# Kernel optimization log

Measured on AMD Instinct MI355X. Metric: run time of the kernel, lower is better.

Reference implementation:

```python
import jax, jax.numpy as jnp
import numpy as np

IN_FEATURES = 8192
OUT_FEATURES = 8192
NNZ = 671088  # in*out*(1-0.99)
BATCH = 1024


def setup_inputs() -> dict:
    key = jax.random.key(0)
    kx, kv, kr, kc = jax.random.split(key, 4)
    x = jax.random.normal(kx, (BATCH, IN_FEATURES), dtype=jnp.float32)
    # values initialized ~ N(0,1) / sqrt(in_features), matching the module
    values = jax.random.normal(kv, (NNZ,), dtype=jnp.float32) * (1.0 / np.sqrt(IN_FEATURES))
    bias = jnp.zeros((OUT_FEATURES,), dtype=jnp.float32)
    rows = jax.random.randint(kr, (NNZ,), 0, IN_FEATURES, dtype=jnp.int32)
    cols = jax.random.randint(kc, (NNZ,), 0, OUT_FEATURES, dtype=jnp.int32)
    return {"x": x, "values": values, "bias": bias, "rows": rows, "cols": cols}


def reference(x, values, bias, rows, cols):
    # Materialize the sparse (in, out) weight via scatter-add.
    # Duplicate (row, col) pairs sum, matching torch COO .coalesce().
    W = jnp.zeros((IN_FEATURES, OUT_FEATURES), dtype=values.dtype)
    W = W.at[rows, cols].add(values)
    # res = addmm(bias, x, W) == x @ W + bias
    return x @ W + bias[None, :]
```

## Files before the change

kernel.cpp:

```cpp
#include <hip/hip_runtime.h>
#include <stdint.h>

#define IN_F   8192
#define OUT_F  8192
#define BATCH  1024
#define BT     8
#define NBT    (BATCH / BT)
#define MAIN_THREADS 1024
#define GROUPS_PER_WAVE 4
#define L_PREF 160
#define XTILE_BYTES (IN_F * 16)

#define NBUCKET 1024
#define P1_THREADS 1024
#define P1_PER 8
#define P1_CHUNK (P1_THREADS * P1_PER)
#define P2_THREADS 1024
#define BIN_STRIDE (L_PREF + 1)

#if __has_builtin(__builtin_amdgcn_fdot2) && __has_builtin(__builtin_amdgcn_perm)
#define USE_DOT2 1
typedef _Float16 half2v __attribute__((ext_vector_type(2)));
#else
#define USE_DOT2 0
#endif

typedef float f32x2 __attribute__((ext_vector_type(2)));


__device__ __forceinline__ unsigned f32_to_bf16_bits_rne(float f) {
    union { float f; unsigned u; } v; v.f = f;
    unsigned u = v.u;
    unsigned r = u + 0x7FFFu + ((u >> 16) & 1u);
    return r >> 16;
}
__device__ __forceinline__ float bf16_hi_bits_to_f32(unsigned b) {
    union { unsigned u; float f; } v; v.u = b & 0xFFFF0000u; return v.f;
}
__device__ __forceinline__ f32x2 unpack_pair(unsigned u) {
    union { unsigned u; float f; } lo, hi;
    lo.u = u << 16; hi.u = u & 0xFFFF0000u;
    f32x2 r; r.x = lo.f; r.y = hi.f; return r;
}

#if USE_DOT2
__device__ __forceinline__ unsigned val_bits(float f) {
    return (unsigned)__builtin_bit_cast(unsigned short, (_Float16)f);
}
__device__ __forceinline__ unsigned x_bits(float f) {
    return (unsigned)__builtin_bit_cast(unsigned short, (_Float16)f);
}
#else
__device__ __forceinline__ unsigned val_bits(float f) { return f32_to_bf16_bits_rne(f); }
__device__ __forceinline__ unsigned x_bits(float f)   { return f32_to_bf16_bits_rne(f); }
#endif

__global__ __launch_bounds__(P1_THREADS) void bin_kernel(
        const int* __restrict__ rows, const int* __restrict__ cols,
        const float* __restrict__ vals,
        int* __restrict__ bcnt, unsigned* __restrict__ ell, int nnz, int L) {
    __shared__ int lcnt[NBUCKET];
    __shared__ int lbase[NBUCKET];
    __shared__ int gbase[NBUCKET];
    __shared__ int wsum[16];
    __shared__ unsigned stage[P1_CHUNK];
    __shared__ unsigned short smap[P1_CHUNK];

    int tid = threadIdx.x;
    int i0 = blockIdx.x * P1_CHUNK;
    lcnt[tid] = 0;
    __syncthreads();

    unsigned mypk[P1_PER];
    int      myb[P1_PER];
    int      myrk[P1_PER];
#pragma unroll
    for (int k = 0; k < P1_PER; ++k) {
        int i = i0 + k * P1_THREADS + tid;
        myb[k] = -1;
        mypk[k] = 0;
        myrk[k] = 0;
        if (i < nnz) {
            int c = cols[i];
            mypk[k] = (val_bits(vals[i]) << 16) | ((unsigned)rows[i] << 3) | ((unsigned)c & 7u);
            myb[k] = c >> 3;
            myrk[k] = atomicAdd(&lcnt[c >> 3], 1);
        }
    }
    __syncthreads();

    {
        int wv = tid >> 6, ln = tid & 63;
        int v = lcnt[tid];
        int sc = v;
#pragma unroll
        for (int off = 1; off < 64; off <<= 1) {
            int o = __shfl_up(sc, off, 64);
            if (ln >= off) sc += o;
        }
        if (ln == 63) wsum[wv] = sc;
        __syncthreads();
        if (tid < 16) {
            int s = wsum[tid];
            int sl = s;
#pragma unroll
            for (int off = 1; off < 16; off <<= 1) {
                int o = __shfl_up(sl, off, 16);
                if (tid >= off) sl += o;
            }
            wsum[tid] = sl - s;
        }
        __syncthreads();
        lbase[tid] = sc - v + wsum[wv];
    }
    __syncthreads();

    {
        int lc = lcnt[tid];
        gbase[tid] = lc ? atomicAdd(&bcnt[tid], lc) : 0;
    }
#pragma unroll
    for (int k = 0; k < P1_PER; ++k) {
        if (myb[k] >= 0) {
            int pos = lbase[myb[k]] + myrk[k];
            stage[pos] = mypk[k];
            smap[pos] = (unsigned short)myb[k];
        }
    }
    __syncthreads();

    int total = lbase[NBUCKET - 1] + lcnt[NBUCKET - 1];
    int cap = 8 * L;
    for (int i = tid; i < total; i += P1_THREADS) {
        int b = smap[i];
        int idx = gbase[b] + (i - lbase[b]);
        if (idx < cap)
            ell[(size_t)b * cap + idx] = stage[i];
    }
}

__global__ __launch_bounds__(P2_THREADS) void build_kernel(
        const int* __restrict__ bcnt, unsigned* __restrict__ ell,
        int* __restrict__ counts, int L) {
    __shared__ unsigned bins[64 * BIN_STRIDE];
    __shared__ int ccnt[64];
    __shared__ int qsh;
    int g = blockIdx.x;
    int tid = threadIdx.x;
    for (int i = tid; i < 64 * BIN_STRIDE; i += P2_THREADS) bins[i] = 0;
    if (tid < 64) ccnt[tid] = 0;
    __syncthreads();

    unsigned* slab = ell + (size_t)g * (64 * L);
    int cap = 8 * L;
#pragma unroll 1
    for (int q = 0; q < 8; ++q) {
        int cb = bcnt[g * 8 + q];
        if (cb > cap) cb = cap;
        const unsigned* bp = slab + q * cap;
        for (int i = tid; i < cb; i += P2_THREADS) {
            unsigned e = bp[i];
            int c64 = q * 8 + (int)(e & 7u);
            int rk = atomicAdd(&ccnt[c64], 1);
            if (rk < L) bins[c64 * BIN_STRIDE + rk] = e;
        }
    }
    __syncthreads();

    if (tid < 64) {
        int c = ccnt[tid];
        counts[g * 64 + tid] = c;
        int mc = min(c, L);
#pragma unroll
        for (int off = 32; off; off >>= 1) mc = max(mc, __shfl_xor(mc, off, 64));
        if (tid == 0) qsh = (mc + 3) >> 2;
    }
    __syncthreads();

    int D = qsh << 8;
    for (int d = tid; d < D; d += P2_THREADS) {
        int q = d >> 8, r = d & 255;
        slab[d] = bins[(r >> 2) * BIN_STRIDE + q * 4 + (r & 3)];
    }
}

#if USE_DOT2
__device__ __forceinline__ void process_pair8(unsigned pk0, unsigned pk1, const char* xbase,
        float& a0, float& a1, float& a2, float& a3,
        float& a4, float& a5, float& a6, float& a7) {
    unsigned off0 = pk0 & 0xFFF8u;
    unsigned off1 = pk1 & 0xFFF8u;
    uint4 q0 = *(const uint4*)(xbase + off0 * 2);
    uint4 q1 = *(const uint4*)(xbase + off1 * 2);
    unsigned vv = __builtin_amdgcn_perm(pk1, pk0, 0x07060302u);
    half2v vh = __builtin_bit_cast(half2v, vv);
    unsigned e0 = __builtin_amdgcn_perm(q1.x, q0.x, 0x05040100u);
    unsigned o0 = __builtin_amdgcn_perm(q1.x, q0.x, 0x07060302u);
    unsigned e1 = __builtin_amdgcn_perm(q1.y, q0.y, 0x05040100u);
    unsigned o1 = __builtin_amdgcn_perm(q1.y, q0.y, 0x07060302u);
    unsigned e2 = __builtin_amdgcn_perm(q1.z, q0.z, 0x05040100u);
    unsigned o2 = __builtin_amdgcn_perm(q1.z, q0.z, 0x07060302u);
    unsigned e3 = __builtin_amdgcn_perm(q1.w, q0.w, 0x05040100u);
    unsigned o3 = __builtin_amdgcn_perm(q1.w, q0.w, 0x07060302u);
    a0 = __builtin_amdgcn_fdot2(__builtin_bit_cast(half2v, e0), vh, a0, false);
    a1 = __builtin_amdgcn_fdot2(__builtin_bit_cast(half2v, o0), vh, a1, false);
    a2 = __builtin_amdgcn_fdot2(__builtin_bit_cast(half2v, e1), vh, a2, false);
    a3 = __builtin_amdgcn_fdot2(__builtin_bit_cast(half2v, o1), vh, a3, false);
    a4 = __builtin_amdgcn_fdot2(__builtin_bit_cast(half2v, e2), vh, a4, false);
    a5 = __builtin_amdgcn_fdot2(__builtin_bit_cast(half2v, o2), vh, a5, false);
    a6 = __builtin_amdgcn_fdot2(__builtin_bit_cast(half2v, e3), vh, a6, false);
    a7 = __builtin_amdgcn_fdot2(__builtin_bit_cast(half2v, o3), vh, a7, false);
}
#else
__device__ __forceinline__ void process_entry8(unsigned pk, const char* xbase,
                                               f32x2& a01, f32x2& a23, f32x2& a45, f32x2& a67) {
    float val = bf16_hi_bits_to_f32(pk);
    f32x2 vv; vv.x = val; vv.y = val;
    unsigned off = pk & 0xFFF8u;
    uint4 d = *(const uint4*)(xbase + off * 2);
    a01 = __builtin_elementwise_fma(unpack_pair(d.x), vv, a01);
    a23 = __builtin_elementwise_fma(unpack_pair(d.y), vv, a23);
    a45 = __builtin_elementwise_fma(unpack_pair(d.z), vv, a45);
    a67 = __builtin_elementwise_fma(unpack_pair(d.w), vv, a67);
}
#endif

__global__ __launch_bounds__(MAIN_THREADS) void spmm_kernel(
        const float* __restrict__ x,
        const float* __restrict__ bias,
        const int* __restrict__ counts,
        const unsigned* __restrict__ ell,
        float* __restrict__ out, int L) {
    extern __shared__ uint4 xl[];
    int w = blockIdx.x;
    int bt = w >> 1;
    int half = w & 1;
    int t = threadIdx.x;
    int b0 = bt * BT;

    for (int r = t; r < IN_F; r += MAIN_THREADS) {
        unsigned u0 = x_bits(x[(b0 + 0) * IN_F + r]);
        unsigned u1 = x_bits(x[(b0 + 1) * IN_F + r]);
        unsigned u2 = x_bits(x[(b0 + 2) * IN_F + r]);
        unsigned u3 = x_bits(x[(b0 + 3) * IN_F + r]);
        unsigned u4 = x_bits(x[(b0 + 4) * IN_F + r]);
        unsigned u5 = x_bits(x[(b0 + 5) * IN_F + r]);
        unsigned u6 = x_bits(x[(b0 + 6) * IN_F + r]);
        unsigned u7 = x_bits(x[(b0 + 7) * IN_F + r]);
        uint4 d;
        d.x = (u1 << 16) | u0;
        d.y = (u3 << 16) | u2;
        d.z = (u5 << 16) | u4;
        d.w = (u7 << 16) | u6;
        xl[r] = d;
    }
    __syncthreads();

    const char* xbase = (const char*)xl;
    int wave = t >> 6;
    int lane = t & 63;
    int n4cap = L >> 2;

#pragma unroll 1
    for (int it = 0; it < GROUPS_PER_WAVE; ++it) {
        int g = half * 64 + wave * GROUPS_PER_WAVE + it;
        int col = (g << 6) + lane;
        int cnt = counts[col];
#pragma unroll
        for (int off = 32; off; off >>= 1) cnt = max(cnt, __shfl_xor(cnt, off, 64));
        int n4 = (cnt + 3) >> 2;
        n4 = min(n4, n4cap);
        const uint4* ep = (const uint4*)(ell + (size_t)g * (L * 64));
        float bv = bias[col];
#if USE_DOT2
        float a0 = 0.f, a1 = 0.f, a2 = 0.f, a3 = 0.f;
        float a4 = 0.f, a5 = 0.f, a6 = 0.f, a7 = 0.f;
        if (n4 > 0) {
            uint4 q = ep[lane];
#pragma unroll 1
            for (int s4 = 1; s4 < n4; ++s4) {
                uint4 qn = ep[s4 * 64 + lane];
                process_pair8(q.x, q.y, xbase, a0, a1, a2, a3, a4, a5, a6, a7);
                process_pair8(q.z, q.w, xbase, a0, a1, a2, a3, a4, a5, a6, a7);
                q = qn;
            }
            process_pair8(q.x, q.y, xbase, a0, a1, a2, a3, a4, a5, a6, a7);
            process_pair8(q.z, q.w, xbase, a0, a1, a2, a3, a4, a5, a6, a7);
        }
        out[(size_t)(b0 + 0) * OUT_F + col] = a0 + bv;
        out[(size_t)(b0 + 1) * OUT_F + col] = a1 + bv;
        out[(size_t)(b0 + 2) * OUT_F + col] = a2 + bv;
        out[(size_t)(b0 + 3) * OUT_F + col] = a3 + bv;
        out[(size_t)(b0 + 4) * OUT_F + col] = a4 + bv;
        out[(size_t)(b0 + 5) * OUT_F + col] = a5 + bv;
        out[(size_t)(b0 + 6) * OUT_F + col] = a6 + bv;
        out[(size_t)(b0 + 7) * OUT_F + col] = a7 + bv;
#else
        f32x2 a01 = {0.f, 0.f}, a23 = {0.f, 0.f}, a45 = {0.f, 0.f}, a67 = {0.f, 0.f};
        if (n4 > 0) {
            uint4 q = ep[lane];
#pragma unroll 1
            for (int s4 = 1; s4 < n4; ++s4) {
                uint4 qn = ep[s4 * 64 + lane];
                process_entry8(q.x, xbase, a01, a23, a45, a67);
                process_entry8(q.y, xbase, a01, a23, a45, a67);
                process_entry8(q.z, xbase, a01, a23, a45, a67);
                process_entry8(q.w, xbase, a01, a23, a45, a67);
                q = qn;
            }
            process_entry8(q.x, xbase, a01, a23, a45, a67);
            process_entry8(q.y, xbase, a01, a23, a45, a67);
            process_entry8(q.z, xbase, a01, a23, a45, a67);
            process_entry8(q.w, xbase, a01, a23, a45, a67);
        }
        out[(size_t)(b0 + 0) * OUT_F + col] = a01.x + bv;
        out[(size_t)(b0 + 1) * OUT_F + col] = a01.y + bv;
        out[(size_t)(b0 + 2) * OUT_F + col] = a23.x + bv;
        out[(size_t)(b0 + 3) * OUT_F + col] = a23.y + bv;
        out[(size_t)(b0 + 4) * OUT_F + col] = a45.x + bv;
        out[(size_t)(b0 + 5) * OUT_F + col] = a45.y + bv;
        out[(size_t)(b0 + 6) * OUT_F + col] = a67.x + bv;
        out[(size_t)(b0 + 7) * OUT_F + col] = a67.y + bv;
#endif
    }
}

extern "C" void kernel_launch(void* const* d_in, const int* in_sizes, int n_in,
                              void* d_out, int out_size, void* d_ws, size_t ws_size,
                              hipStream_t stream) {
    const float* x      = (const float*)d_in[0];
    const float* values = (const float*)d_in[1];
    const float* bias   = (const float*)d_in[2];
    const int* rows = (const int*)d_in[3];
    const int* cols = (const int*)d_in[4];
    float* out = (float*)d_out;
    int nnz = in_sizes[1];

    int* bcnt   = (int*)d_ws;
    int* counts = bcnt + NBUCKET;
    unsigned* ell = (unsigned*)(counts + 8192);

    long long cap_slots = ((long long)(ws_size / 4) - (NBUCKET + 8192)) / 8192;
    int L = (int)(cap_slots & ~3LL);
    if (L > L_PREF) L = L_PREF;
    if (L < 4) L = 4;

    static int attr_set = -1;
    if (attr_set < 0) {
        hipFuncSetAttribute((const void*)spmm_kernel,
                            hipFuncAttributeMaxDynamicSharedMemorySize, XTILE_BYTES);
        attr_set = 1;
    }

    hipMemsetAsync(bcnt, 0, NBUCKET * 4, stream);
    int nb1 = (nnz + P1_CHUNK - 1) / P1_CHUNK;
    bin_kernel<<<nb1, P1_THREADS, 0, stream>>>(rows, cols, values, bcnt, ell, nnz, L);
    build_kernel<<<128, P2_THREADS, 0, stream>>>(bcnt, ell, counts, L);
    spmm_kernel<<<NBT * 2, MAIN_THREADS, XTILE_BYTES, stream>>>(x, bias, counts, ell, out, L);
}
```

Before: 162.1 us.

## Sub-bucket sort ELL entries by row bits in build kernel, halve partition chunk

The build kernel now makes two passes over each bucket: the first counts entries per column and 3-bit sub-bucket of the packed row offset, then a prefix order is computed with a per-column rotation, and the second pass scatters entries into bins at sorted positions. This partially orders each column's nonzeros by row region, which should improve locality of x-tile reads in the main SpMM kernel, and the rotation staggers concurrent columns across different regions. It doubles the global reads and shared atomics in the build step. The partition chunk per thread is also halved, which gives more blocks with less work each.

```diff
diff --git a/kernel.cpp b/kernel.cpp
--- a/kernel.cpp
+++ b/kernel.cpp
@@ -13,7 +13,7 @@
 
 #define NBUCKET 1024
 #define P1_THREADS 1024
-#define P1_PER 8
+#define P1_PER 4
 #define P1_CHUNK (P1_THREADS * P1_PER)
 #define P2_THREADS 1024
 #define BIN_STRIDE (L_PREF + 1)
@@ -143,16 +143,18 @@
         const int* __restrict__ bcnt, unsigned* __restrict__ ell,
         int* __restrict__ counts, int L) {
     __shared__ unsigned bins[64 * BIN_STRIDE];
-    __shared__ int ccnt[64];
+    __shared__ int scnt[64 * 8];
+    __shared__ int soff[64 * 8];
     __shared__ int qsh;
     int g = blockIdx.x;
     int tid = threadIdx.x;
     for (int i = tid; i < 64 * BIN_STRIDE; i += P2_THREADS) bins[i] = 0;
-    if (tid < 64) ccnt[tid] = 0;
+    if (tid < 512) scnt[tid] = 0;
     __syncthreads();
 
     unsigned* slab = ell + (size_t)g * (64 * L);
     int cap = 8 * L;
+
 #pragma unroll 1
     for (int q = 0; q < 8; ++q) {
         int cb = bcnt[g * 8 + q];
@@ -161,19 +163,44 @@
         for (int i = tid; i < cb; i += P2_THREADS) {
             unsigned e = bp[i];
             int c64 = q * 8 + (int)(e & 7u);
-            int rk = atomicAdd(&ccnt[c64], 1);
-            if (rk < L) bins[c64 * BIN_STRIDE + rk] = e;
+            int sb = (int)((e >> 3) & 7u);
+            atomicAdd(&scnt[c64 * 8 + sb], 1);
         }
     }
     __syncthreads();
 
     if (tid < 64) {
-        int c = ccnt[tid];
-        counts[g * 64 + tid] = c;
-        int mc = min(c, L);
-#pragma unroll
-        for (int off = 32; off; off >>= 1) mc = max(mc, __shfl_xor(mc, off, 64));
+        int rot = tid & 7;
+        int off = 0;
+#pragma unroll
+        for (int k = 0; k < 8; ++k) {
+            int sb = (k + rot) & 7;
+            soff[tid * 8 + sb] = off;
+            off += scnt[tid * 8 + sb];
+        }
+        counts[g * 64 + tid] = off;
+        int mc = min(off, L);
+#pragma unroll
+        for (int o = 32; o; o >>= 1) mc = max(mc, __shfl_xor(mc, o, 64));
         if (tid == 0) qsh = (mc + 3) >> 2;
+#pragma unroll
+        for (int k = 0; k < 8; ++k) scnt[tid * 8 + k] = 0;
+    }
+    __syncthreads();
+
+#pragma unroll 1
+    for (int q = 0; q < 8; ++q) {
+        int cb = bcnt[g * 8 + q];
+        if (cb > cap) cb = cap;
+        const unsigned* bp = slab + q * cap;
+        for (int i = tid; i < cb; i += P2_THREADS) {
+            unsigned e = bp[i];
+            int c64 = q * 8 + (int)(e & 7u);
+            int sb = (int)((e >> 3) & 7u);
+            int rk = atomicAdd(&scnt[c64 * 8 + sb], 1);
+            int pos = soff[c64 * 8 + sb] + rk;
+            if (pos < L) bins[c64 * BIN_STRIDE + pos] = e;
+        }
     }
     __syncthreads();
 
```

Result: no change. 163.1 us (+0.6%).
